# Kernel optimization log

Hardware: AMD Instinct MI355X
Metric: run time of the kernel (lower is better)

## Reference

```python
import jax, jax.numpy as jnp
import numpy as np

EMBED_DIM = 768
NUM_HEADS = 12
HEAD_DIM = EMBED_DIM // NUM_HEADS
MAX_REL = 50
B, L = 4, 1024


def setup_inputs() -> dict:
    key = jax.random.key(0)
    ks = jax.random.split(key, 8)
    query = jax.random.normal(ks[0], (B, L, EMBED_DIM), dtype=jnp.float32)
    k_in = jax.random.normal(ks[1], (B, L, EMBED_DIM), dtype=jnp.float32)
    v_in = jax.random.normal(ks[2], (B, L, EMBED_DIM), dtype=jnp.float32)
    # monotone float timestamps per batch (arange fill)
    patch_indices = jnp.arange(B * L, dtype=jnp.float32).reshape(B, L)
    std = 1.0 / np.sqrt(EMBED_DIM)
    in_proj_w = jax.random.normal(ks[3], (3 * EMBED_DIM, EMBED_DIM), dtype=jnp.float32) * std
    in_proj_b = jnp.zeros((3 * EMBED_DIM,), dtype=jnp.float32)
    out_proj_w = jax.random.normal(ks[4], (EMBED_DIM, EMBED_DIM), dtype=jnp.float32) * std
    out_proj_b = jnp.zeros((EMBED_DIM,), dtype=jnp.float32)
    rel_bias = jax.random.truncated_normal(ks[5], -2.0, 2.0, (NUM_HEADS, 2 * MAX_REL + 1), dtype=jnp.float32) * 0.1
    return {"query": query, "key": k_in, "value": v_in, "patch_indices": patch_indices,
            "in_proj_w": in_proj_w, "in_proj_b": in_proj_b,
            "out_proj_w": out_proj_w, "out_proj_b": out_proj_b, "rel_bias": rel_bias}


def _attention(query, patch_indices, in_proj_w, in_proj_b, out_proj_w, out_proj_b, rel_bias):
    Bq, Lq, D = query.shape
    H, hd, M = NUM_HEADS, HEAD_DIM, MAX_REL
    qkv = query @ in_proj_w.T + in_proj_b            # [B,L,3D]
    q, k, v = jnp.split(qkv, 3, axis=-1)
    q = q.reshape(Bq, Lq, H, hd).transpose(0, 2, 1, 3) * (hd ** -0.5)
    k = k.reshape(Bq, Lq, H, hd).transpose(0, 2, 1, 3)
    v = v.reshape(Bq, Lq, H, hd).transpose(0, 2, 1, 3)
    scores = jnp.einsum('bhld,bhmd->bhlm', q, k)     # [B,H,L,L]
    # sequence-position relative bias
    idxs = jnp.arange(Lq)
    rel_pos = jnp.clip(idxs[None, :] - idxs[:, None], -M, M) + M   # [L,L]
    scores = scores + rel_bias[:, rel_pos][None]                   # [1,H,L,L]
    # data-dependent relative-time bias
    deltas = patch_indices[:, 1:] - patch_indices[:, :-1]          # [B,L-1]
    dt = jnp.nanmedian(deltas, axis=1)
    dt = jnp.where(jnp.isfinite(dt) & (dt > 0), dt, 1.0)[:, None, None]
    rel_time = patch_indices[:, :, None] - patch_indices[:, None, :]  # [B,L,L]
    invalid = jnp.isnan(rel_time) | (rel_time < -M) | (rel_time > M)
    rel_time = jnp.where(invalid, 0.0, rel_time)
    rel_idx = (jnp.clip(jnp.round(rel_time / dt), -M, M) + M).astype(jnp.int32)  # [B,L,L]
    bias = jnp.take(rel_bias, rel_idx, axis=1)       # [H,B,L,L]
    scores = scores + jnp.moveaxis(bias, 0, 1)       # [B,H,L,L]
    probs = jax.nn.softmax(scores, axis=-1)
    out = jnp.einsum('bhlm,bhmd->bhld', probs, v)
    out = out.transpose(0, 2, 1, 3).reshape(Bq, Lq, D)
    return out @ out_proj_w.T + out_proj_b


def reference(query, key, value, patch_indices, in_proj_w, in_proj_b, out_proj_w, out_proj_b, rel_bias):
    # NOTE: the original module ignores key/value and builds qkv from query.
    return _attention(query, patch_indices, in_proj_w, in_proj_b, out_proj_w, out_proj_b, rel_bias)
```

## Files before the change

### kernel.cpp

```cpp
#include <hip/hip_runtime.h>
#include <hip/hip_bf16.h>

#define BB 4
#define LL 1024
#define DD 768
#define HH 12
#define HD 64
#define MREL 50
#define NBIAS 101
#define GK 768
#define STR 72
#define BXS 68

#define NEG_INF (-__builtin_inff())

#define QB_F   ((size_t)0)
#define KB_F   ((size_t)1572864)
#define VTB_F  ((size_t)3145728)
#define XBF_F  ((size_t)4718592)
#define WIBF_F ((size_t)6291456)
#define WOBF_F ((size_t)7176192)
#define BIDX_F ((size_t)7471104)
#define DT_F   ((size_t)9568256)

#define NQ4  (BB*LL*DD)
#define NWI4 (3*DD*DD)

typedef __attribute__((ext_vector_type(8)))  short bf16x8;
typedef __attribute__((ext_vector_type(4)))  float f32x4;
typedef __attribute__((ext_vector_type(16))) float f32x16;

__device__ __forceinline__ unsigned short f2bf(float f) {
    unsigned u = __float_as_uint(f);
    u += 0x7fffu + ((u >> 16) & 1u);
    return (unsigned short)(u >> 16);
}

__device__ __forceinline__ void gload_lds16(const void* g, void* l) {
    __builtin_amdgcn_global_load_lds(
        (const __attribute__((address_space(1))) void*)g,
        (__attribute__((address_space(3))) void*)l, 16, 0, 0);
}

__global__ __launch_bounds__(256) void prep_kernel(
    const float* __restrict__ patch, float* __restrict__ dt,
    const float* __restrict__ q, const float* __restrict__ wi, const float* __restrict__ wo,
    unsigned short* __restrict__ qd_, unsigned short* __restrict__ wid,
    unsigned short* __restrict__ wod) {
    int tid = threadIdx.x;
    if (blockIdx.x >= 4) {
        int i = ((blockIdx.x - 4) * 256 + tid) * 4;
        const float* src; unsigned short* dst; int off;
        if (i < NQ4)              { src = q;  dst = qd_; off = i; }
        else if (i < NQ4 + NWI4)  { src = wi; dst = wid; off = i - NQ4; }
        else                      { src = wo; dst = wod; off = i - NQ4 - NWI4; }
        float4 v = *(const float4*)&src[off];
        ushort4 o;
        o.x = f2bf(v.x); o.y = f2bf(v.y); o.z = f2bf(v.z); o.w = f2bf(v.w);
        *(ushort4*)&dst[off] = o;
        return;
    }
    __shared__ __align__(16) float del[1024];
    __shared__ __align__(16) unsigned long long key64[1024];
    __shared__ int nvalid;
    __shared__ float acc;
    int b = blockIdx.x;
    if (tid == 0) { nvalid = 0; acc = 0.f; }
    __syncthreads();
    int cnt = 0;
#pragma unroll
    for (int r = 0; r < 4; ++r) {
        int i = tid + r * 256;
        float v = __builtin_nanf("");
        if (i < LL - 1) {
            v = patch[b * LL + i + 1] - patch[b * LL + i];
            if (v == v) ++cnt;
        }
        del[i] = v;
        unsigned bits = (v == v) ? __float_as_uint(v) : 0x7FC00000u;
        unsigned ordk = (bits & 0x80000000u) ? ~bits : (bits | 0x80000000u);
        key64[i] = ((unsigned long long)ordk << 10) | (unsigned)i;
    }
    atomicAdd(&nvalid, cnt);
    __syncthreads();
    int i0 = tid, i1 = tid + 256, i2 = tid + 512, i3 = tid + 768;
    float v0 = del[i0], v1 = del[i1], v2 = del[i2], v3 = del[i3];
    unsigned long long k0 = key64[i0], k1 = key64[i1], k2 = key64[i2], k3 = key64[i3];
    int c0 = 0, c1 = 0, c2 = 0, c3 = 0;
#define CMPK(kx) { unsigned long long _k = (kx); \
    c0 += (_k < k0) ? 1 : 0; c1 += (_k < k1) ? 1 : 0; \
    c2 += (_k < k2) ? 1 : 0; c3 += (_k < k3) ? 1 : 0; }
    for (int j = 0; j < 1024; j += 8) {
        ulonglong2 a = *(const ulonglong2*)&key64[j];
        ulonglong2 bq = *(const ulonglong2*)&key64[j + 2];
        ulonglong2 cq = *(const ulonglong2*)&key64[j + 4];
        ulonglong2 dq = *(const ulonglong2*)&key64[j + 6];
        CMPK(a.x); CMPK(a.y); CMPK(bq.x); CMPK(bq.y);
        CMPK(cq.x); CMPK(cq.y); CMPK(dq.x); CMPK(dq.y);
    }
#undef CMPK
    int n = nvalid;
#define FIN(vr, cr) if (vr == vr) { \
    if (n & 1) { if (cr == n / 2) atomicAdd(&acc, vr); } \
    else { if (cr == n / 2 - 1 || cr == n / 2) atomicAdd(&acc, 0.5f * vr); } }
    FIN(v0, c0); FIN(v1, c1); FIN(v2, c2); FIN(v3, c3);
#undef FIN
    __syncthreads();
    if (tid == 0) {
        float m = acc;
        float res = (n > 0 && m == m && fabsf(m) != __builtin_inff() && m > 0.f) ? m : 1.0f;
        dt[b] = res;
    }
}

__global__ __launch_bounds__(256) void bidx_kernel(const float* __restrict__ patch,
                                                   const float* __restrict__ dtb,
                                                   unsigned short* __restrict__ bidx) {
    int flat = (blockIdx.x * 256 + threadIdx.x) * 8;
    int b = flat >> 20;
    int rem = flat & 1048575;
    int i = rem >> 10;
    int j0 = rem & 1023;
    float pi = patch[b * LL + i];
    float inv_dt = 1.0f / dtb[b];
    float4 pa = *(const float4*)&patch[b * LL + j0];
    float4 pb4 = *(const float4*)&patch[b * LL + j0 + 4];
    unsigned out[4];
#define MK(pj, jofs, dst, shift) { \
    int d = (j0 + jofs) - i; d = d < -MREL ? -MREL : (d > MREL ? MREL : d); \
    float rt = pi - (pj); \
    if (!(rt == rt) || rt < -(float)MREL || rt > (float)MREL) rt = 0.f; \
    float fr = fminf(fmaxf(rintf(rt * inv_dt), -(float)MREL), (float)MREL); \
    unsigned u = (unsigned)(d + MREL) | (((unsigned)((int)fr + MREL)) << 8); \
    dst |= (u << shift); }
    unsigned t;
    t = 0; MK(pa.x, 0, t, 0); MK(pa.y, 1, t, 16); out[0] = t;
    t = 0; MK(pa.z, 2, t, 0); MK(pa.w, 3, t, 16); out[1] = t;
    t = 0; MK(pb4.x, 4, t, 0); MK(pb4.y, 5, t, 16); out[2] = t;
    t = 0; MK(pb4.z, 6, t, 0); MK(pb4.w, 7, t, 16); out[3] = t;
#undef MK
    *(uint4*)&bidx[flat] = *(uint4*)&out[0];
}

#define GEMM_CORE(TN_, RB_, NT_)                                               \
    __shared__ unsigned short As[64 * 64];                                     \
    __shared__ unsigned short Bs[TN_ * 64];                                    \
    int tid = threadIdx.x;                                                     \
    int m0 = blockIdx.x << 6, n0 = blockIdx.y * TN_;                           \
    int lane = tid & 63, w = tid >> 6;                                         \
    int wn = w * (TN_ / 4);                                                    \
    int srow = tid >> 3, scol = (tid & 7) << 3;                                \
    const unsigned short* Ag = Ab + (size_t)(m0 + srow) * GK + scol;           \
    const unsigned short* Bg = Wb + (size_t)(n0 + srow) * GK + scol;           \
    f32x4 acc[4][NT_];                                                         \
    _Pragma("unroll") for (int i = 0; i < 4; ++i)                              \
        _Pragma("unroll") for (int j = 0; j < NT_; ++j)                        \
            acc[i][j] = (f32x4){0.f, 0.f, 0.f, 0.f};                           \
    int qd_ = lane >> 4;                                                       \
    int rA = lane & 15, rB = wn + (lane & 15);                                 \
    for (int kc = 0; kc < GK; kc += 64) {                                      \
        __syncthreads();                                                       \
        _Pragma("unroll") for (int r = 0; r < 2; ++r)                          \
            gload_lds16(Ag + (size_t)(r * 32) * GK + kc, As + tid * 8 + r * 2048); \
        _Pragma("unroll") for (int r = 0; r < RB_; ++r)                        \
            gload_lds16(Bg + (size_t)(r * 32) * GK + kc, Bs + tid * 8 + r * 2048); \
        __syncthreads();                                                       \
        _Pragma("unroll") for (int ks = 0; ks < 2; ++ks) {                     \
            bf16x8 af[4], bfr[NT_];                                            \
            _Pragma("unroll") for (int t = 0; t < 4; ++t)                      \
                af[t] = *(const bf16x8*)&As[(rA + t * 16) * 64 + ks * 32 + qd_ * 8]; \
            _Pragma("unroll") for (int t = 0; t < NT_; ++t)                    \
                bfr[t] = *(const bf16x8*)&Bs[(rB + t * 16) * 64 + ks * 32 + qd_ * 8]; \
            _Pragma("unroll") for (int i = 0; i < 4; ++i)                      \
                _Pragma("unroll") for (int j = 0; j < NT_; ++j)                \
                    acc[i][j] = __builtin_amdgcn_mfma_f32_16x16x32_bf16(       \
                        af[i], bfr[j], acc[i][j], 0, 0, 0);                    \
        }                                                                      \
    }                                                                          \
    int colL = lane & 15, rq = lane >> 4;

__global__ __launch_bounds__(256) void qkv_gemm(
    const unsigned short* __restrict__ Ab, const unsigned short* __restrict__ Wb,
    const float* __restrict__ bias,
    unsigned short* __restrict__ qb, unsigned short* __restrict__ kb,
    unsigned short* __restrict__ vtb) {
    GEMM_CORE(128, 4, 2);
    int sec = n0 / DD;
    float scale = (sec == 0) ? 0.125f : 1.0f;
#pragma unroll
    for (int j = 0; j < 2; ++j) {
        int n = n0 + wn + j * 16 + colL;
        int d768 = n - sec * DD;
        int hh = d768 >> 6, dd = d768 & 63;
        float bn = bias[n];
#pragma unroll
        for (int i = 0; i < 4; ++i) {
            int rowb = m0 + i * 16 + rq * 4;
#pragma unroll
            for (int r = 0; r < 4; ++r) {
                int m = rowb + r;
                int bidx = m >> 10, l = m & 1023;
                unsigned short val = f2bf((acc[i][j][r] + bn) * scale);
                if (sec == 0)
                    qb[(((size_t)bidx * HH + hh) * LL + l) * HD + dd] = val;
                else if (sec == 1)
                    kb[(((size_t)bidx * HH + hh) * LL + l) * HD + dd] = val;
                else
                    vtb[(((size_t)bidx * HH + hh) * HD + dd) * LL + l] = val;
            }
        }
    }
}

__global__ __launch_bounds__(256) void out_gemm(
    const unsigned short* __restrict__ Ab, const unsigned short* __restrict__ Wb,
    const float* __restrict__ bias, float* __restrict__ C) {
    GEMM_CORE(64, 2, 1);
    {
        int n = n0 + wn + colL;
        float bn = bias[n];
#pragma unroll
        for (int i = 0; i < 4; ++i) {
            int rowb = m0 + i * 16 + rq * 4;
#pragma unroll
            for (int r = 0; r < 4; ++r)
                C[(size_t)(rowb + r) * DD + n] = acc[i][0][r] + bn;
        }
    }
}

__global__ __launch_bounds__(256) void attn_kernel(
    const unsigned short* __restrict__ QB, const unsigned short* __restrict__ KB,
    const unsigned short* __restrict__ VTB, const unsigned short* __restrict__ BIDX,
    const float* __restrict__ relb, unsigned short* __restrict__ aout) {
    __shared__ unsigned short Ks[64 * STR];
    __shared__ unsigned short Vt[64 * STR];
    __shared__ unsigned short Ps[64 * STR];
    __shared__ unsigned short Bxs[64 * BXS];
    __shared__ float sb[NBIAS];
    __shared__ float psum_s[128];
    __shared__ float linv_s[64];
    int tid = threadIdx.x;
    int w = tid >> 6, lane = tid & 63, li = lane & 31, qd = lane >> 5;
    int jt = w & 1, it = w >> 1;
    int bh = blockIdx.x, b = bh / HH, h = bh - b * HH;
    int q0 = blockIdx.y << 6;
    if (tid < NBIAS) sb[tid] = relb[h * NBIAS + tid];
    int i_loc = it * 32 + li;
    int i_abs = q0 + i_loc;
    bf16x8 kq[4];
    const unsigned short* qrow = QB + ((size_t)bh * LL + i_abs) * HD + qd * 8;
#pragma unroll
    for (int ks = 0; ks < 4; ++ks) kq[ks] = *(const bf16x8*)(qrow + ks * 16);
    float l_run = 0.f;
    f32x16 O;
#pragma unroll
    for (int r = 0; r < 16; ++r) O[r] = 0.f;
    int srow = tid >> 3, sc = (tid & 7) << 3;
    const unsigned short* kgb = KB + (size_t)bh * LL * HD;
    const unsigned short* vgb = VTB + (size_t)bh * HD * LL;
    const unsigned short* bxg = BIDX + ((size_t)b << 20) + (size_t)q0 * 1024;
    bf16x8 kvr[2], vvr[2], bxr[2];
#pragma unroll
    for (int rep = 0; rep < 2; ++rep) {
        int r = srow + rep * 32;
        kvr[rep] = *(const bf16x8*)(kgb + (size_t)r * HD + sc);
        vvr[rep] = *(const bf16x8*)(vgb + (size_t)r * LL + sc);
        bxr[rep] = *(const bf16x8*)(bxg + (size_t)r * 1024 + sc);
    }
    for (int kt = 0; kt < 16; ++kt) {
        __syncthreads();
#pragma unroll
        for (int rep = 0; rep < 2; ++rep) {
            int r = srow + rep * 32;
            *(bf16x8*)&Ks[r * STR + sc] = kvr[rep];
            *(bf16x8*)&Vt[r * STR + sc] = vvr[rep];
            *(bf16x8*)&Bxs[r * BXS + sc] = bxr[rep];
        }
        if (kt + 1 < 16) {
#pragma unroll
            for (int rep = 0; rep < 2; ++rep) {
                int r = srow + rep * 32;
                kvr[rep] = *(const bf16x8*)(kgb + (size_t)((kt + 1) * 64 + r) * HD + sc);
                vvr[rep] = *(const bf16x8*)(vgb + (size_t)r * LL + (kt + 1) * 64 + sc);
                bxr[rep] = *(const bf16x8*)(bxg + (size_t)r * 1024 + (kt + 1) * 64 + sc);
            }
        }
        __syncthreads();
        f32x16 st;
#pragma unroll
        for (int r = 0; r < 16; ++r) st[r] = 0.f;
#pragma unroll
        for (int ks = 0; ks < 4; ++ks) {
            bf16x8 ak = *(const bf16x8*)&Ks[(jt * 32 + li) * STR + ks * 16 + qd * 8];
            st = __builtin_amdgcn_mfma_f32_32x32x16_bf16(ak, kq[ks], st, 0, 0, 0);
        }
#pragma unroll
        for (int g4 = 0; g4 < 4; ++g4) {
            ushort4 bi = *(const ushort4*)&Bxs[i_loc * BXS + jt * 32 + g4 * 8 + qd * 4];
#pragma unroll
            for (int q = 0; q < 4; ++q) {
                int r = g4 * 4 + q;
                unsigned u = (q == 0) ? bi.x : (q == 1) ? bi.y : (q == 2) ? bi.z : bi.w;
                st[r] = st[r] + sb[u & 0xffu] + sb[u >> 8];
            }
        }
        float rs = 0.f;
        unsigned pu[8];
#pragma unroll
        for (int pr = 0; pr < 8; ++pr) {
            float p0 = __expf(st[2 * pr]);
            float p1 = __expf(st[2 * pr + 1]);
            unsigned u0 = __float_as_uint(p0);
            u0 += 0x7fffu + ((u0 >> 16) & 1u); u0 &= 0xffff0000u;
            unsigned u1 = __float_as_uint(p1);
            u1 += 0x7fffu + ((u1 >> 16) & 1u); u1 &= 0xffff0000u;
            rs += __uint_as_float(u0);
            rs += __uint_as_float(u1);
            pu[pr] = (u0 >> 16) | u1;
        }
        rs += __shfl_xor(rs, 32);
        l_run += rs;
#pragma unroll
        for (int pr = 0; pr < 8; ++pr) {
            int r = pr * 2;
            int jl = (r & 3) + ((r >> 2) << 3) + (qd << 2);
            *(unsigned*)&Ps[i_loc * STR + jt * 32 + jl] = pu[pr];
        }
        __syncthreads();
#pragma unroll
        for (int ks = 0; ks < 4; ++ks) {
            bf16x8 ap = *(const bf16x8*)&Ps[i_loc * STR + ks * 16 + qd * 8];
            bf16x8 bv = *(const bf16x8*)&Vt[(jt * 32 + li) * STR + ks * 16 + qd * 8];
            O = __builtin_amdgcn_mfma_f32_32x32x16_bf16(ap, bv, O, 0, 0, 0);
        }
    }
    if (qd == 0) psum_s[jt * 64 + i_loc] = l_run;
    __syncthreads();
    if (jt == 0 && qd == 0)
        linv_s[i_loc] = 1.0f / (psum_s[i_loc] + psum_s[64 + i_loc]);
    __syncthreads();
#pragma unroll
    for (int r = 0; r < 16; ++r) {
        int row = (r & 3) + ((r >> 2) << 3) + (qd << 2);
        float v = O[r] * linv_s[it * 32 + row];
        aout[(size_t)(b * LL + q0 + it * 32 + row) * DD + h * HD + jt * 32 + li] = f2bf(v);
    }
}

extern "C" void kernel_launch(void* const* d_in, const int* in_sizes, int n_in,
                              void* d_out, int out_size, void* d_ws, size_t ws_size,
                              hipStream_t stream) {
    const float* query    = (const float*)d_in[0];
    const float* patch    = (const float*)d_in[3];
    const float* in_w     = (const float*)d_in[4];
    const float* in_b     = (const float*)d_in[5];
    const float* out_w    = (const float*)d_in[6];
    const float* out_b    = (const float*)d_in[7];
    const float* rel_bias = (const float*)d_in[8];
    float* ws  = (float*)d_ws;
    float* out = (float*)d_out;

    unsigned short* qb   = (unsigned short*)(ws + QB_F);
    unsigned short* kb   = (unsigned short*)(ws + KB_F);
    unsigned short* vtb  = (unsigned short*)(ws + VTB_F);
    unsigned short* xbf  = (unsigned short*)(ws + XBF_F);
    unsigned short* wibf = (unsigned short*)(ws + WIBF_F);
    unsigned short* wobf = (unsigned short*)(ws + WOBF_F);
    unsigned short* bidx = (unsigned short*)(ws + BIDX_F);

    prep_kernel<<<5380, 256, 0, stream>>>(patch, ws + DT_F, query, in_w, out_w,
                                          xbf, wibf, wobf);
    bidx_kernel<<<2048, 256, 0, stream>>>(patch, ws + DT_F, bidx);
    qkv_gemm<<<dim3(64, 18), 256, 0, stream>>>(xbf, wibf, in_b, qb, kb, vtb);
    attn_kernel<<<dim3(BB * HH, LL / 64), 256, 0, stream>>>(
        qb, kb, vtb, bidx, rel_bias, xbf);
    out_gemm<<<dim3(64, 12), 256, 0, stream>>>(xbf, wobf, out_b, out);
}
```

Before: 212.0 us.

## Keep P in registers via permlane swap, use exp2 and band-skip bias

The attention kernel no longer writes probabilities to LDS and adds a block barrier to read them back. Each wave repacks its P fragment with permlane32_swap into the MFMA A-operand layout and accumulates a partial O over its own 32 keys. The two key-half waves then combine their partial outputs through LDS at the end. Log2(e) is folded into the Q scale and the bias table so exp2 replaces expf, and packing uses v_cvt_pk_bf16_f32 instead of manual rounding. Tiles far from the diagonal also skip the positional-bias lookup by using a constant clipped value. The cost is twice the O accumulator registers and an extra reduction step in the epilogue.

```diff
diff --git a/kernel.cpp b/kernel.cpp
--- a/kernel.cpp
+++ b/kernel.cpp
@@ -29,6 +29,7 @@
 typedef __attribute__((ext_vector_type(8)))  short bf16x8;
 typedef __attribute__((ext_vector_type(4)))  float f32x4;
 typedef __attribute__((ext_vector_type(16))) float f32x16;
+typedef __attribute__((ext_vector_type(4)))  unsigned int u32x4;
 
 __device__ __forceinline__ unsigned short f2bf(float f) {
     unsigned u = __float_as_uint(f);
@@ -186,7 +187,7 @@
     unsigned short* __restrict__ vtb) {
     GEMM_CORE(128, 4, 2);
     int sec = n0 / DD;
-    float scale = (sec == 0) ? 0.125f : 1.0f;
+    float scale = (sec == 0) ? 0.18033688011112042f : 1.0f;
 #pragma unroll
     for (int j = 0; j < 2; ++j) {
         int n = n0 + wn + j * 16 + colL;
@@ -233,19 +234,21 @@
     const unsigned short* __restrict__ QB, const unsigned short* __restrict__ KB,
     const unsigned short* __restrict__ VTB, const unsigned short* __restrict__ BIDX,
     const float* __restrict__ relb, unsigned short* __restrict__ aout) {
-    __shared__ unsigned short Ks[64 * STR];
-    __shared__ unsigned short Vt[64 * STR];
-    __shared__ unsigned short Ps[64 * STR];
-    __shared__ unsigned short Bxs[64 * BXS];
+    __shared__ __align__(16) unsigned short smem[2 * 64 * STR + 64 * BXS];
     __shared__ float sb[NBIAS];
     __shared__ float psum_s[128];
     __shared__ float linv_s[64];
+    unsigned short* Ks  = smem;
+    unsigned short* Vt  = smem + 64 * STR;
+    unsigned short* Bxs = smem + 2 * 64 * STR;
+    float* fcomb = (float*)smem;
+
     int tid = threadIdx.x;
     int w = tid >> 6, lane = tid & 63, li = lane & 31, qd = lane >> 5;
     int jt = w & 1, it = w >> 1;
     int bh = blockIdx.x, b = bh / HH, h = bh - b * HH;
     int q0 = blockIdx.y << 6;
-    if (tid < NBIAS) sb[tid] = relb[h * NBIAS + tid];
+    if (tid < NBIAS) sb[tid] = relb[h * NBIAS + tid] * 1.44269504088896340736f;
     int i_loc = it * 32 + li;
     int i_abs = q0 + i_loc;
     bf16x8 kq[4];
@@ -253,9 +256,9 @@
 #pragma unroll
     for (int ks = 0; ks < 4; ++ks) kq[ks] = *(const bf16x8*)(qrow + ks * 16);
     float l_run = 0.f;
-    f32x16 O;
-#pragma unroll
-    for (int r = 0; r < 16; ++r) O[r] = 0.f;
+    f32x16 O0, O1;
+#pragma unroll
+    for (int r = 0; r < 16; ++r) { O0[r] = 0.f; O1[r] = 0.f; }
     int srow = tid >> 3, sc = (tid & 7) << 3;
     const unsigned short* kgb = KB + (size_t)bh * LL * HD;
     const unsigned short* vgb = VTB + (size_t)bh * HD * LL;
@@ -268,6 +271,8 @@
         vvr[rep] = *(const bf16x8*)(vgb + (size_t)r * LL + sc);
         bxr[rep] = *(const bf16x8*)(bxg + (size_t)r * 1024 + sc);
     }
+    __syncthreads();
+    float sb0 = sb[0], sb100 = sb[100];
     for (int kt = 0; kt < 16; ++kt) {
         __syncthreads();
 #pragma unroll
@@ -295,56 +300,90 @@
             bf16x8 ak = *(const bf16x8*)&Ks[(jt * 32 + li) * STR + ks * 16 + qd * 8];
             st = __builtin_amdgcn_mfma_f32_32x32x16_bf16(ak, kq[ks], st, 0, 0, 0);
         }
-#pragma unroll
-        for (int g4 = 0; g4 < 4; ++g4) {
-            ushort4 bi = *(const ushort4*)&Bxs[i_loc * BXS + jt * 32 + g4 * 8 + qd * 4];
-#pragma unroll
-            for (int q = 0; q < 4; ++q) {
-                int r = g4 * 4 + q;
-                unsigned u = (q == 0) ? bi.x : (q == 1) ? bi.y : (q == 2) ? bi.z : bi.w;
-                st[r] = st[r] + sb[u & 0xffu] + sb[u >> 8];
+        int delta = (kt << 6) + (jt << 5) - q0 - (it << 5);
+        if (delta >= 81 || delta <= -81) {
+            float db = (delta >= 81) ? sb100 : sb0;
+#pragma unroll
+            for (int g4 = 0; g4 < 4; ++g4) {
+                ushort4 bi = *(const ushort4*)&Bxs[i_loc * BXS + jt * 32 + g4 * 8 + qd * 4];
+#pragma unroll
+                for (int q = 0; q < 4; ++q) {
+                    int r = g4 * 4 + q;
+                    unsigned u = (q == 0) ? bi.x : (q == 1) ? bi.y : (q == 2) ? bi.z : bi.w;
+                    st[r] = st[r] + db + sb[u >> 8];
+                }
             }
+        } else {
+#pragma unroll
+            for (int g4 = 0; g4 < 4; ++g4) {
+                ushort4 bi = *(const ushort4*)&Bxs[i_loc * BXS + jt * 32 + g4 * 8 + qd * 4];
+#pragma unroll
+                for (int q = 0; q < 4; ++q) {
+                    int r = g4 * 4 + q;
+                    unsigned u = (q == 0) ? bi.x : (q == 1) ? bi.y : (q == 2) ? bi.z : bi.w;
+                    st[r] = st[r] + sb[u & 0xffu] + sb[u >> 8];
+                }
+            }
         }
         float rs = 0.f;
-        unsigned pu[8];
+        unsigned W[8];
 #pragma unroll
         for (int pr = 0; pr < 8; ++pr) {
-            float p0 = __expf(st[2 * pr]);
-            float p1 = __expf(st[2 * pr + 1]);
-            unsigned u0 = __float_as_uint(p0);
-            u0 += 0x7fffu + ((u0 >> 16) & 1u); u0 &= 0xffff0000u;
-            unsigned u1 = __float_as_uint(p1);
-            u1 += 0x7fffu + ((u1 >> 16) & 1u); u1 &= 0xffff0000u;
-            rs += __uint_as_float(u0);
-            rs += __uint_as_float(u1);
-            pu[pr] = (u0 >> 16) | u1;
+            float p0 = __builtin_amdgcn_exp2f(st[2 * pr]);
+            float p1 = __builtin_amdgcn_exp2f(st[2 * pr + 1]);
+            rs += p0 + p1;
+            unsigned wpk;
+            asm("v_cvt_pk_bf16_f32 %0, %1, %2" : "=v"(wpk) : "v"(p0), "v"(p1));
+            W[pr] = wpk;
         }
         rs += __shfl_xor(rs, 32);
         l_run += rs;
-#pragma unroll
-        for (int pr = 0; pr < 8; ++pr) {
-            int r = pr * 2;
-            int jl = (r & 3) + ((r >> 2) << 3) + (qd << 2);
-            *(unsigned*)&Ps[i_loc * STR + jt * 32 + jl] = pu[pr];
-        }
-        __syncthreads();
-#pragma unroll
-        for (int ks = 0; ks < 4; ++ks) {
-            bf16x8 ap = *(const bf16x8*)&Ps[i_loc * STR + ks * 16 + qd * 8];
-            bf16x8 bv = *(const bf16x8*)&Vt[(jt * 32 + li) * STR + ks * 16 + qd * 8];
-            O = __builtin_amdgcn_mfma_f32_32x32x16_bf16(ap, bv, O, 0, 0, 0);
+        auto s02 = __builtin_amdgcn_permlane32_swap(W[0], W[2], false, false);
+        auto s13 = __builtin_amdgcn_permlane32_swap(W[1], W[3], false, false);
+        auto s46 = __builtin_amdgcn_permlane32_swap(W[4], W[6], false, false);
+        auto s57 = __builtin_amdgcn_permlane32_swap(W[5], W[7], false, false);
+        u32x4 a0w = {(unsigned)s02[0], (unsigned)s13[0], (unsigned)s02[1], (unsigned)s13[1]};
+        u32x4 a1w = {(unsigned)s46[0], (unsigned)s57[0], (unsigned)s46[1], (unsigned)s57[1]};
+        bf16x8 ap0 = __builtin_bit_cast(bf16x8, a0w);
+        bf16x8 ap1 = __builtin_bit_cast(bf16x8, a1w);
+        {
+            bf16x8 bv;
+            bv = *(const bf16x8*)&Vt[(li) * STR + jt * 32 + qd * 8];
+            O0 = __builtin_amdgcn_mfma_f32_32x32x16_bf16(ap0, bv, O0, 0, 0, 0);
+            bv = *(const bf16x8*)&Vt[(li) * STR + jt * 32 + 16 + qd * 8];
+            O0 = __builtin_amdgcn_mfma_f32_32x32x16_bf16(ap1, bv, O0, 0, 0, 0);
+            bv = *(const bf16x8*)&Vt[(32 + li) * STR + jt * 32 + qd * 8];
+            O1 = __builtin_amdgcn_mfma_f32_32x32x16_bf16(ap0, bv, O1, 0, 0, 0);
+            bv = *(const bf16x8*)&Vt[(32 + li) * STR + jt * 32 + 16 + qd * 8];
+            O1 = __builtin_amdgcn_mfma_f32_32x32x16_bf16(ap1, bv, O1, 0, 0, 0);
         }
     }
     if (qd == 0) psum_s[jt * 64 + i_loc] = l_run;
     __syncthreads();
     if (jt == 0 && qd == 0)
         linv_s[i_loc] = 1.0f / (psum_s[i_loc] + psum_s[64 + i_loc]);
-    __syncthreads();
-#pragma unroll
-    for (int r = 0; r < 16; ++r) {
-        int row = (r & 3) + ((r >> 2) << 3) + (qd << 2);
-        float v = O[r] * linv_s[it * 32 + row];
-        aout[(size_t)(b * LL + q0 + it * 32 + row) * DD + h * HD + jt * 32 + li] = f2bf(v);
+    if (jt == 1) {
+        int ibase = it * 32;
+#pragma unroll
+        for (int r = 0; r < 16; ++r) {
+            int irow = (r & 3) + ((r >> 2) << 3) + (qd << 2);
+            fcomb[(ibase + irow) * 64 + li] = O0[r];
+            fcomb[(ibase + irow) * 64 + 32 + li] = O1[r];
+        }
+    }
+    __syncthreads();
+    if (jt == 0) {
+        int ibase = it * 32;
+#pragma unroll
+        for (int r = 0; r < 16; ++r) {
+            int irow = (r & 3) + ((r >> 2) << 3) + (qd << 2);
+            float inv = linv_s[ibase + irow];
+            float v0 = (O0[r] + fcomb[(ibase + irow) * 64 + li]) * inv;
+            float v1 = (O1[r] + fcomb[(ibase + irow) * 64 + 32 + li]) * inv;
+            size_t rowoff = (size_t)(b * LL + q0 + ibase + irow) * DD + h * HD;
+            aout[rowoff + li] = f2bf(v0);
+            aout[rowoff + 32 + li] = f2bf(v1);
+        }
     }
 }
 
```

New measurement: 203.8 us. 3.8% less time.
